# Kernel tuning notes

Hardware: AMD Instinct MI355X
Metric: run time of the kernel (lower is better)

## Reference

```python
import jax, jax.numpy as jnp
import numpy as np
import math

EMBED = 1024
HEADS = 16
HEAD_DIM = EMBED // HEADS


def setup_inputs() -> dict:
    key = jax.random.key(0)
    ks = jax.random.split(key, 9)
    B, S = 2, 2048
    query = jax.random.normal(ks[0], (B, S, EMBED), dtype=jnp.float32)
    key_t = jax.random.normal(ks[1], (B, S, EMBED), dtype=jnp.float32)
    value = jax.random.normal(ks[2], (B, S, EMBED), dtype=jnp.float32)
    mask = jax.random.randint(ks[3], (B, 1, S, S), 0, 2, dtype=jnp.int32)
    # nn.Linear(head_dim, head_dim, bias=False) weights: [out, in]
    sc = 1.0 / math.sqrt(HEAD_DIM)
    Wq = jax.random.uniform(ks[4], (HEAD_DIM, HEAD_DIM), jnp.float32, -sc, sc)
    Wk = jax.random.uniform(ks[5], (HEAD_DIM, HEAD_DIM), jnp.float32, -sc, sc)
    Wv = jax.random.uniform(ks[6], (HEAD_DIM, HEAD_DIM), jnp.float32, -sc, sc)
    so = 1.0 / math.sqrt(EMBED)
    Wo = jax.random.uniform(ks[7], (EMBED, EMBED), jnp.float32, -so, so)
    bo = jax.random.uniform(ks[8], (EMBED,), jnp.float32, -so, so)
    return {"query": query, "key": key_t, "value": value, "mask": mask,
            "Wq": Wq, "Wk": Wk, "Wv": Wv, "Wo": Wo, "bo": bo}


def reference(query, key, value, mask, Wq, Wk, Wv, Wo, bo):
    B, Sq, E = query.shape
    Sk = key.shape[1]
    H, D = HEADS, HEAD_DIM
    # Faithful raw reshape into heads (as in the torch source, no transpose)
    q = query.reshape(B, H, Sq, D)
    k = key.reshape(B, H, Sk, D)
    v = value.reshape(B, H, Sk, D)
    # per-head_dim Linear (bias-free): x @ W.T
    Q = jnp.einsum('bhsd,ed->bhse', q, Wq)
    K = jnp.einsum('bhsd,ed->bhse', k, Wk)
    V = jnp.einsum('bhsd,ed->bhse', v, Wv)
    scores = jnp.einsum('bhqd,bhkd->bhqk', Q, K)  # [B,H,Sq,Sk]
    scores = jnp.where(mask == 0, jnp.float32(-1e20), scores)
    # NOTE: source divides by sqrt(embed_size), not sqrt(head_dim)
    attn = jax.nn.softmax(scores / jnp.float32(math.sqrt(E)), axis=-1)
    out = jnp.einsum('bhqk,bhkd->bhqd', attn, V).reshape(B, Sq, H * D)
    return out @ Wo.T + bo
```

## Files before the change

kernel.cpp:

```cpp
#include <hip/hip_runtime.h>

typedef __attribute__((ext_vector_type(8))) short short8;
typedef __attribute__((ext_vector_type(4))) float f32x4;
typedef __attribute__((ext_vector_type(2))) int int2v;
typedef __attribute__((ext_vector_type(4))) int int4v;

__device__ __forceinline__ short f2bf(float f) {
  unsigned u = __builtin_bit_cast(unsigned, f);
  u += 0x7fff + ((u >> 16) & 1);
  return (short)(u >> 16);
}

__device__ __forceinline__ int pk2bf(float lo, float hi) {
#if defined(__gfx950__) && __has_builtin(__builtin_amdgcn_cvt_pk_bf16_f32)
  typedef __attribute__((ext_vector_type(2))) __bf16 bf16x2;
  bf16x2 v = __builtin_amdgcn_cvt_pk_bf16_f32(lo, hi);
  return __builtin_bit_cast(int, v);
#else
  return (int)(unsigned short)(short)f2bf(lo) | (((int)f2bf(hi)) << 16);
#endif
}

__device__ __forceinline__ short8 pack8(f32x4 a, f32x4 b) {
  int4v t;
  t.x = pk2bf(a[0], a[1]);
  t.y = pk2bf(a[2], a[3]);
  t.z = pk2bf(b[0], b[1]);
  t.w = pk2bf(b[2], b[3]);
  return __builtin_bit_cast(short8, t);
}

__device__ __forceinline__ float fand(float p, int m) {
  return __builtin_bit_cast(float, __builtin_bit_cast(int, p) & m);
}

__device__ __forceinline__ int bmask(unsigned nib, int bit) {
#if __has_builtin(__builtin_amdgcn_sbfe)
  return __builtin_amdgcn_sbfe((int)nib, bit, 1);
#else
  return -(int)((nib >> bit) & 1);
#endif
}

__device__ __forceinline__ float fexp2(float x) {
#if __has_builtin(__builtin_amdgcn_exp2f)
  return __builtin_amdgcn_exp2f(x);
#else
  return exp2f(x);
#endif
}

__device__ __forceinline__ void glds16(const short* g, short* lbase, int lane) {
#if __has_builtin(__builtin_amdgcn_global_load_lds)
  __builtin_amdgcn_global_load_lds(
      (const __attribute__((address_space(1))) unsigned int*)g,
      (__attribute__((address_space(3))) unsigned int*)lbase, 16, 0, 0);
#else
  *(short8*)(lbase + lane * 8) = *(const short8*)g;
#endif
}

__global__ __launch_bounds__(256) void prep(const float* __restrict__ q,
                                            const float* __restrict__ k,
                                            const float* __restrict__ v,
                                            const float* __restrict__ Wq,
                                            const float* __restrict__ Wk,
                                            const float* __restrict__ Wv,
                                            const float* __restrict__ Wo,
                                            const int* __restrict__ mask,
                                            short* __restrict__ Qp,
                                            short* __restrict__ Kp,
                                            short* __restrict__ Vtp,
                                            short* __restrict__ Wob,
                                            unsigned long long* __restrict__ mpk) {
  const int bid = blockIdx.x;
  const int tid = threadIdx.x;

  if (bid >= 4096) {
#pragma unroll
    for (int it = 0; it < 4; ++it) {
      const int gid = ((bid - 4096) * 4 + it) * 256 + tid;
      const int base = gid & ~63, j = gid & 63;
      const int val = mask[base + ((j & 3) << 4) + (j >> 2)];
      const unsigned long long bal = __ballot(val != 0);
      if (j == 0) mpk[gid >> 6] = bal;
    }
    return;
  }
  if (bid >= 3072) {
    const int i = ((bid - 3072) * 256 + tid) * 4;
    const f32x4 x = *(const f32x4*)&Wo[i];
    int2v o;
    o.x = pk2bf(x[0], x[1]);
    o.y = pk2bf(x[2], x[3]);
    *(int2v*)&Wob[i] = o;
    return;
  }

  __shared__ short xt[64][72];
  __shared__ short ot[64][72];
  const int mode = bid >> 10;
  const int bt = bid & 1023;
  const float* X;
  const float* W;
  float scale;
  if (mode == 0) { X = q; W = Wq; scale = 0.045084220f; }
  else if (mode == 1) { X = k; W = Wk; scale = 1.0f; }
  else { X = v; W = Wv; scale = 1.0f; }

  const int r0 = bt * 64;
  const int row = tid >> 2, seg = (tid & 3) * 16;
  const f32x4* xs = (const f32x4*)(X + (r0 + row) * 64 + seg);
  const f32x4 x0 = xs[0], x1 = xs[1], x2 = xs[2], x3 = xs[3];
  *(short8*)&xt[row][seg] = pack8(x0, x1);
  *(short8*)&xt[row][seg + 8] = pack8(x2, x3);
  __syncthreads();

  const int lane = tid & 63, wave = tid >> 6;
  const int m16 = lane & 15, quad = lane >> 4;

  const short8 a0 = *(const short8*)&xt[wave * 16 + m16][quad * 8];
  const short8 a1 = *(const short8*)&xt[wave * 16 + m16][32 + quad * 8];

  f32x4 acc[4];
#pragma unroll
  for (int nt = 0; nt < 4; ++nt) {
    const f32x4* wp0 = (const f32x4*)&W[(nt * 16 + m16) * 64 + quad * 8];
    const f32x4* wp1 = (const f32x4*)&W[(nt * 16 + m16) * 64 + 32 + quad * 8];
    const short8 b0 = pack8(wp0[0], wp0[1]);
    const short8 b1 = pack8(wp1[0], wp1[1]);
    f32x4 z = (f32x4){0.f, 0.f, 0.f, 0.f};
    z = __builtin_amdgcn_mfma_f32_16x16x32_bf16(a0, b0, z, 0, 0, 0);
    z = __builtin_amdgcn_mfma_f32_16x16x32_bf16(a1, b1, z, 0, 0, 0);
    acc[nt] = z;
  }

  if (mode != 2) {
#pragma unroll
    for (int nt = 0; nt < 4; ++nt)
#pragma unroll
      for (int r = 0; r < 4; ++r)
        ot[wave * 16 + quad * 4 + r][nt * 16 + m16] = f2bf(acc[nt][r] * scale);
  } else {
#pragma unroll
    for (int nt = 0; nt < 4; ++nt)
#pragma unroll
      for (int r = 0; r < 4; ++r)
        ot[nt * 16 + m16][16 * quad + 4 * r + wave] = f2bf(acc[nt][r]);
  }
  __syncthreads();

  const int orow = tid >> 2, opart = tid & 3;
  if (mode != 2) {
    short* dst = (mode == 0 ? Qp : Kp) + (r0 + orow) * 64 + opart * 16;
    *(short8*)&dst[0] = *(const short8*)&ot[orow][opart * 16];
    *(short8*)&dst[8] = *(const short8*)&ot[orow][opart * 16 + 8];
  } else {
    const int bh = r0 >> 11, s0 = r0 & 2047;
    short* dst = Vtp + bh * 131072 + orow * 2048 + s0 + opart * 16;
    *(short8*)&dst[0] = *(const short8*)&ot[orow][opart * 16];
    *(short8*)&dst[8] = *(const short8*)&ot[orow][opart * 16 + 8];
  }
}

__global__ __launch_bounds__(512) void flash2(const short* __restrict__ Qp,
                                              const short* __restrict__ Kp,
                                              const short* __restrict__ Vt,
                                              const unsigned long long* __restrict__ mpk,
                                              short* __restrict__ O) {
  __shared__ __attribute__((aligned(16))) short kv[4][4096];
  __shared__ __attribute__((aligned(16))) short pt[2][128][72];
  __shared__ float lbuf[128];
  const int tid = threadIdx.x;
  const int bid = blockIdx.x;
  const int local = bid >> 3;
  const int bh = (bid & 7) * 4 + (local >> 4);
  const int q0 = (local & 15) << 7;
  const int b = bh >> 4;
  const short* Qh = Qp + bh * 131072;
  const short* Kh = Kp + bh * 131072;
  const short* Vh = Vt + bh * 131072;
  const int lane = tid & 63, wave = tid >> 6;
  const int half = wave >> 2, wq = wave & 3;
  const int m16 = lane & 15, quad = lane >> 4;
  const int srow = lane >> 3, sj = (lane & 7) ^ srow;
  const int msh = m16 * 4;
  const int koff = m16 * 128 + ((quad ^ (m16 & 7)) * 16);
  short* ktb = &kv[half * 2][0];
  short* vtb = &kv[half * 2 + 1][0];
  const int tsel = wq >> 1, rbase = (wq & 1) * 32;

  short8 aq[2][2];
#pragma unroll
  for (int g = 0; g < 2; ++g)
#pragma unroll
    for (int h = 0; h < 2; ++h)
      aq[g][h] = *(const short8*)&Qh[(q0 + wq * 32 + g * 16 + m16) * 64 + h * 32 + quad * 8];

  const unsigned long long* mq = mpk + (b * 2048 + q0 + wq * 32 + quad * 4) * 32;

  float l[2][4];
  f32x4 oacc[2][4];
#pragma unroll
  for (int g = 0; g < 2; ++g)
#pragma unroll
    for (int r = 0; r < 4; ++r) l[g][r] = 0.f;
#pragma unroll
  for (int g = 0; g < 2; ++g)
#pragma unroll
    for (int dt = 0; dt < 4; ++dt) oacc[g][dt] = (f32x4){0.f, 0.f, 0.f, 0.f};

  for (int i = 0; i < 16; ++i) {
    const int ka = half * 16 + i;
    const int k0 = ka << 6;
    __syncthreads();
#pragma unroll
    for (int t = 0; t < 4; ++t) {
      const int crow = rbase + t * 8;
      if (tsel == 0)
        glds16(Kh + (k0 + crow + srow) * 64 + sj * 8, ktb + crow * 64, lane);
      else
        glds16(Vh + (crow + srow) * 2048 + k0 + sj * 8, vtb + crow * 64, lane);
    }
    __syncthreads();

    f32x4 s[2][4];
#pragma unroll
    for (int nt = 0; nt < 4; ++nt) {
      const int o0 = nt * 2048 + koff;
      const short8 kb0 = *(const short8*)((const char*)ktb + o0);
      const short8 kb1 = *(const short8*)((const char*)ktb + (o0 ^ 64));
#pragma unroll
      for (int g = 0; g < 2; ++g) {
        f32x4 z = (f32x4){0.f, 0.f, 0.f, 0.f};
        z = __builtin_amdgcn_mfma_f32_16x16x32_bf16(aq[g][0], kb0, z, 0, 0, 0);
        z = __builtin_amdgcn_mfma_f32_16x16x32_bf16(aq[g][1], kb1, z, 0, 0, 0);
        s[g][nt] = z;
      }
    }

#pragma unroll
    for (int g = 0; g < 2; ++g) {
#pragma unroll
      for (int r = 0; r < 4; ++r) {
        const unsigned long long w = mq[g * 512 + r * 32 + ka];
        const unsigned nib = (unsigned)(w >> msh) & 15u;
        const float p0 = fand(fexp2(s[g][0][r]), bmask(nib, 0));
        const float p1 = fand(fexp2(s[g][1][r]), bmask(nib, 1));
        const float p2 = fand(fexp2(s[g][2][r]), bmask(nib, 2));
        const float p3 = fand(fexp2(s[g][3][r]), bmask(nib, 3));
        l[g][r] += (p0 + p1) + (p2 + p3);
        int2v pp;
        pp.x = pk2bf(p0, p1);
        pp.y = pk2bf(p2, p3);
        *(int2v*)&pt[half][wq * 32 + g * 16 + quad * 4 + r][msh] = pp;
      }
    }

    short8 ap[2][2];
#pragma unroll
    for (int g = 0; g < 2; ++g)
#pragma unroll
      for (int h = 0; h < 2; ++h)
        ap[g][h] = *(const short8*)&pt[half][wq * 32 + g * 16 + m16][h * 32 + quad * 8];

#pragma unroll
    for (int dt = 0; dt < 4; ++dt) {
      const int o0 = dt * 2048 + koff;
      const short8 vb0 = *(const short8*)((const char*)vtb + o0);
      const short8 vb1 = *(const short8*)((const char*)vtb + (o0 ^ 64));
#pragma unroll
      for (int g = 0; g < 2; ++g) {
        f32x4 z = oacc[g][dt];
        z = __builtin_amdgcn_mfma_f32_16x16x32_bf16(ap[g][0], vb0, z, 0, 0, 0);
        z = __builtin_amdgcn_mfma_f32_16x16x32_bf16(ap[g][1], vb1, z, 0, 0, 0);
        oacc[g][dt] = z;
      }
    }
  }

#pragma unroll
  for (int g = 0; g < 2; ++g)
#pragma unroll
    for (int r = 0; r < 4; ++r)
#pragma unroll
      for (int off = 1; off < 16; off <<= 1) l[g][r] += __shfl_xor(l[g][r], off, 16);

  __syncthreads();

  if (half == 1) {
    float* obuf = (float*)kv;
#pragma unroll
    for (int g = 0; g < 2; ++g)
#pragma unroll
      for (int r = 0; r < 4; ++r) {
        const int row = wq * 32 + g * 16 + quad * 4 + r;
#pragma unroll
        for (int dt = 0; dt < 4; ++dt) obuf[row * 64 + dt * 16 + m16] = oacc[g][dt][r];
        if (m16 == 0) lbuf[row] = l[g][r];
      }
  }
  __syncthreads();

  if (half == 0) {
    const float* obuf = (const float*)kv;
#pragma unroll
    for (int g = 0; g < 2; ++g)
#pragma unroll
      for (int r = 0; r < 4; ++r) {
        const int row = wq * 32 + g * 16 + quad * 4 + r;
        const float inv = 1.0f / (l[g][r] + lbuf[row]);
#pragma unroll
        for (int dt = 0; dt < 4; ++dt)
          pt[0][row][dt * 16 + m16] =
              f2bf((oacc[g][dt][r] + obuf[row * 64 + dt * 16 + m16]) * inv);
      }
    const int orow = lane >> 1, opart = lane & 1;
    const int prow = wq * 32 + orow;
    short* og = O + (bh * 2048 + q0 + prow) * 64 + opart * 32;
#pragma unroll
    for (int c = 0; c < 32; c += 8)
      *(short8*)&og[c] = *(const short8*)&pt[0][prow][opart * 32 + c];
  }
}

__global__ __launch_bounds__(256) void outproj(const short* __restrict__ Ob,
                                               const short* __restrict__ Wob,
                                               const float* __restrict__ bo,
                                               float* __restrict__ out) {
  __shared__ short at[64][72];
  __shared__ short bt[128][72];
  const int tid = threadIdx.x;
  const int bid = blockIdx.x;
  const int ct = bid >> 6, rt = bid & 63;
  const int r0 = rt * 64, c0 = ct * 128;
  const int lane = tid & 63, wave = tid >> 6;
  const int mr = (wave >> 1) * 32, nc = (wave & 1) * 64;
  const int m16 = lane & 15, quad = lane >> 4;
  const int arow = tid >> 2, apart = tid & 3;
  const int brow = tid >> 1, bhalf = (tid & 1) * 32;

  f32x4 acc[2][4];
#pragma unroll
  for (int mt = 0; mt < 2; ++mt)
#pragma unroll
    for (int nt = 0; nt < 4; ++nt) acc[mt][nt] = (f32x4){0.f, 0.f, 0.f, 0.f};

  for (int kc = 0; kc < 16; ++kc) {
    __syncthreads();
    const short* ag = &Ob[(r0 + arow) * 1024 + kc * 64 + apart * 16];
    const short* bg = &Wob[(c0 + brow) * 1024 + kc * 64 + bhalf];
    *(short8*)&at[arow][apart * 16] = *(const short8*)&ag[0];
    *(short8*)&at[arow][apart * 16 + 8] = *(const short8*)&ag[8];
    *(short8*)&bt[brow][bhalf] = *(const short8*)&bg[0];
    *(short8*)&bt[brow][bhalf + 8] = *(const short8*)&bg[8];
    *(short8*)&bt[brow][bhalf + 16] = *(const short8*)&bg[16];
    *(short8*)&bt[brow][bhalf + 24] = *(const short8*)&bg[24];
    __syncthreads();

#pragma unroll
    for (int kh = 0; kh < 2; ++kh) {
      short8 af[2], bf[4];
#pragma unroll
      for (int i = 0; i < 2; ++i)
        af[i] = *(const short8*)&at[mr + i * 16 + m16][kh * 32 + quad * 8];
#pragma unroll
      for (int j = 0; j < 4; ++j)
        bf[j] = *(const short8*)&bt[nc + j * 16 + m16][kh * 32 + quad * 8];
#pragma unroll
      for (int mt = 0; mt < 2; ++mt)
#pragma unroll
        for (int nt = 0; nt < 4; ++nt)
          acc[mt][nt] = __builtin_amdgcn_mfma_f32_16x16x32_bf16(af[mt], bf[nt], acc[mt][nt], 0, 0, 0);
    }
  }

#pragma unroll
  for (int nt = 0; nt < 4; ++nt) {
    const int col = c0 + nc + nt * 16 + m16;
    const float bias = bo[col];
#pragma unroll
    for (int mt = 0; mt < 2; ++mt)
#pragma unroll
      for (int rr = 0; rr < 4; ++rr)
        out[(r0 + mr + mt * 16 + quad * 4 + rr) * 1024 + col] = acc[mt][nt][rr] + bias;
  }
}

extern "C" void kernel_launch(void* const* d_in, const int* in_sizes, int n_in,
                              void* d_out, int out_size, void* d_ws, size_t ws_size,
                              hipStream_t stream) {
  const float* query = (const float*)d_in[0];
  const float* key = (const float*)d_in[1];
  const float* value = (const float*)d_in[2];
  const int* mask = (const int*)d_in[3];
  const float* Wq = (const float*)d_in[4];
  const float* Wk = (const float*)d_in[5];
  const float* Wv = (const float*)d_in[6];
  const float* Wo = (const float*)d_in[7];
  const float* bo = (const float*)d_in[8];
  float* out = (float*)d_out;

  char* ws = (char*)d_ws;
  short* Qp = (short*)(ws);
  short* Kp = (short*)(ws + 8388608);
  short* Vt = (short*)(ws + 16777216);
  short* Ob = (short*)(ws + 25165824);
  short* Wob = (short*)(ws + 33554432);
  unsigned long long* mpk = (unsigned long long*)(ws + 35651584);

  prep<<<12288, 256, 0, stream>>>(query, key, value, Wq, Wk, Wv, Wo, mask,
                                  Qp, Kp, Vt, Wob, mpk);
  flash2<<<512, 512, 0, stream>>>(Qp, Kp, Vt, mpk, Ob);
  outproj<<<512, 256, 0, stream>>>(Ob, Wob, bo, out);
}
```

Baseline: 253.4 us.

## Replace split-K flash kernel with double-buffered single-pass 256-thread version

The attention kernel no longer splits the key range across two 4-wave halves of a 512-thread block, which had to merge partial outputs and row sums through shared memory at the end. Each 4-wave block now walks all 32 key tiles itself. The next K/V tile and its mask words are prefetched into a second LDS buffer while the current tile is computed, leaving one barrier per iteration. This removes the cross-half reduction and hides load latency, at the cost of half as many waves per block and a longer serial loop per wave.

```diff
diff --git a/kernel.cpp b/kernel.cpp
--- a/kernel.cpp
+++ b/kernel.cpp
@@ -163,14 +163,14 @@
   }
 }
 
-__global__ __launch_bounds__(512) void flash2(const short* __restrict__ Qp,
+__global__ __launch_bounds__(256) void flashp(const short* __restrict__ Qp,
                                               const short* __restrict__ Kp,
                                               const short* __restrict__ Vt,
                                               const unsigned long long* __restrict__ mpk,
                                               short* __restrict__ O) {
-  __shared__ __attribute__((aligned(16))) short kv[4][4096];
-  __shared__ __attribute__((aligned(16))) short pt[2][128][72];
-  __shared__ float lbuf[128];
+  __shared__ __attribute__((aligned(16))) short kt[2][4096];
+  __shared__ __attribute__((aligned(16))) short vt[2][4096];
+  __shared__ __attribute__((aligned(16))) short pt[128][72];
   const int tid = threadIdx.x;
   const int bid = blockIdx.x;
   const int local = bid >> 3;
@@ -181,23 +181,19 @@
   const short* Kh = Kp + bh * 131072;
   const short* Vh = Vt + bh * 131072;
   const int lane = tid & 63, wave = tid >> 6;
-  const int half = wave >> 2, wq = wave & 3;
   const int m16 = lane & 15, quad = lane >> 4;
   const int srow = lane >> 3, sj = (lane & 7) ^ srow;
   const int msh = m16 * 4;
   const int koff = m16 * 128 + ((quad ^ (m16 & 7)) * 16);
-  short* ktb = &kv[half * 2][0];
-  short* vtb = &kv[half * 2 + 1][0];
-  const int tsel = wq >> 1, rbase = (wq & 1) * 32;
 
   short8 aq[2][2];
 #pragma unroll
   for (int g = 0; g < 2; ++g)
 #pragma unroll
     for (int h = 0; h < 2; ++h)
-      aq[g][h] = *(const short8*)&Qh[(q0 + wq * 32 + g * 16 + m16) * 64 + h * 32 + quad * 8];
-
-  const unsigned long long* mq = mpk + (b * 2048 + q0 + wq * 32 + quad * 4) * 32;
+      aq[g][h] = *(const short8*)&Qh[(q0 + wave * 32 + g * 16 + m16) * 64 + h * 32 + quad * 8];
+
+  const unsigned long long* mq = mpk + (b * 2048 + q0 + wave * 32 + quad * 4) * 32;
 
   float l[2][4];
   f32x4 oacc[2][4];
@@ -210,26 +206,35 @@
 #pragma unroll
     for (int dt = 0; dt < 4; ++dt) oacc[g][dt] = (f32x4){0.f, 0.f, 0.f, 0.f};
 
-  for (int i = 0; i < 16; ++i) {
-    const int ka = half * 16 + i;
-    const int k0 = ka << 6;
+  auto stage = [&](int buf, int ka) {
+#pragma unroll
+    for (int t = 0; t < 2; ++t) {
+      const int crow = wave * 16 + t * 8;
+      glds16(Kh + (ka * 64 + crow + srow) * 64 + sj * 8, &kt[buf][crow * 64], lane);
+      glds16(Vh + (crow + srow) * 2048 + ka * 64 + sj * 8, &vt[buf][crow * 64], lane);
+    }
+  };
+  auto lmask = [&](unsigned long long (&mw)[2][4], int ka) {
+#pragma unroll
+    for (int g = 0; g < 2; ++g)
+#pragma unroll
+      for (int r = 0; r < 4; ++r) mw[g][r] = mq[g * 512 + r * 32 + ka];
+  };
+
+  auto body = [&](int ka, int buf, unsigned long long (&mwU)[2][4],
+                  unsigned long long (&mwN)[2][4]) {
     __syncthreads();
-#pragma unroll
-    for (int t = 0; t < 4; ++t) {
-      const int crow = rbase + t * 8;
-      if (tsel == 0)
-        glds16(Kh + (k0 + crow + srow) * 64 + sj * 8, ktb + crow * 64, lane);
-      else
-        glds16(Vh + (crow + srow) * 2048 + k0 + sj * 8, vtb + crow * 64, lane);
-    }
-    __syncthreads();
+    if (ka < 31) {
+      stage(buf ^ 1, ka + 1);
+      lmask(mwN, ka + 1);
+    }
 
     f32x4 s[2][4];
 #pragma unroll
     for (int nt = 0; nt < 4; ++nt) {
       const int o0 = nt * 2048 + koff;
-      const short8 kb0 = *(const short8*)((const char*)ktb + o0);
-      const short8 kb1 = *(const short8*)((const char*)ktb + (o0 ^ 64));
+      const short8 kb0 = *(const short8*)((const char*)&kt[buf][0] + o0);
+      const short8 kb1 = *(const short8*)((const char*)&kt[buf][0] + (o0 ^ 64));
 #pragma unroll
       for (int g = 0; g < 2; ++g) {
         f32x4 z = (f32x4){0.f, 0.f, 0.f, 0.f};
@@ -243,8 +248,7 @@
     for (int g = 0; g < 2; ++g) {
 #pragma unroll
       for (int r = 0; r < 4; ++r) {
-        const unsigned long long w = mq[g * 512 + r * 32 + ka];
-        const unsigned nib = (unsigned)(w >> msh) & 15u;
+        const unsigned nib = (unsigned)(mwU[g][r] >> msh) & 15u;
         const float p0 = fand(fexp2(s[g][0][r]), bmask(nib, 0));
         const float p1 = fand(fexp2(s[g][1][r]), bmask(nib, 1));
         const float p2 = fand(fexp2(s[g][2][r]), bmask(nib, 2));
@@ -253,7 +257,7 @@
         int2v pp;
         pp.x = pk2bf(p0, p1);
         pp.y = pk2bf(p2, p3);
-        *(int2v*)&pt[half][wq * 32 + g * 16 + quad * 4 + r][msh] = pp;
+        *(int2v*)&pt[wave * 32 + g * 16 + quad * 4 + r][msh] = pp;
       }
     }
 
@@ -262,13 +266,13 @@
     for (int g = 0; g < 2; ++g)
 #pragma unroll
       for (int h = 0; h < 2; ++h)
-        ap[g][h] = *(const short8*)&pt[half][wq * 32 + g * 16 + m16][h * 32 + quad * 8];
+        ap[g][h] = *(const short8*)&pt[wave * 32 + g * 16 + m16][h * 32 + quad * 8];
 
 #pragma unroll
     for (int dt = 0; dt < 4; ++dt) {
       const int o0 = dt * 2048 + koff;
-      const short8 vb0 = *(const short8*)((const char*)vtb + o0);
-      const short8 vb1 = *(const short8*)((const char*)vtb + (o0 ^ 64));
+      const short8 vb0 = *(const short8*)((const char*)&vt[buf][0] + o0);
+      const short8 vb1 = *(const short8*)((const char*)&vt[buf][0] + (o0 ^ 64));
 #pragma unroll
       for (int g = 0; g < 2; ++g) {
         f32x4 z = oacc[g][dt];
@@ -277,51 +281,35 @@
         oacc[g][dt] = z;
       }
     }
+  };
+
+  unsigned long long mwA[2][4], mwB[2][4];
+  stage(0, 0);
+  lmask(mwA, 0);
+
+  for (int kk = 0; kk < 16; ++kk) {
+    body(2 * kk, 0, mwA, mwB);
+    body(2 * kk + 1, 1, mwB, mwA);
   }
 
 #pragma unroll
   for (int g = 0; g < 2; ++g)
 #pragma unroll
-    for (int r = 0; r < 4; ++r)
+    for (int r = 0; r < 4; ++r) {
 #pragma unroll
       for (int off = 1; off < 16; off <<= 1) l[g][r] += __shfl_xor(l[g][r], off, 16);
-
-  __syncthreads();
-
-  if (half == 1) {
-    float* obuf = (float*)kv;
-#pragma unroll
-    for (int g = 0; g < 2; ++g)
-#pragma unroll
-      for (int r = 0; r < 4; ++r) {
-        const int row = wq * 32 + g * 16 + quad * 4 + r;
-#pragma unroll
-        for (int dt = 0; dt < 4; ++dt) obuf[row * 64 + dt * 16 + m16] = oacc[g][dt][r];
-        if (m16 == 0) lbuf[row] = l[g][r];
-      }
-  }
-  __syncthreads();
-
-  if (half == 0) {
-    const float* obuf = (const float*)kv;
-#pragma unroll
-    for (int g = 0; g < 2; ++g)
-#pragma unroll
-      for (int r = 0; r < 4; ++r) {
-        const int row = wq * 32 + g * 16 + quad * 4 + r;
-        const float inv = 1.0f / (l[g][r] + lbuf[row]);
-#pragma unroll
-        for (int dt = 0; dt < 4; ++dt)
-          pt[0][row][dt * 16 + m16] =
-              f2bf((oacc[g][dt][r] + obuf[row * 64 + dt * 16 + m16]) * inv);
-      }
-    const int orow = lane >> 1, opart = lane & 1;
-    const int prow = wq * 32 + orow;
-    short* og = O + (bh * 2048 + q0 + prow) * 64 + opart * 32;
-#pragma unroll
-    for (int c = 0; c < 32; c += 8)
-      *(short8*)&og[c] = *(const short8*)&pt[0][prow][opart * 32 + c];
-  }
+      const float inv = 1.0f / l[g][r];
+#pragma unroll
+      for (int dt = 0; dt < 4; ++dt)
+        pt[wave * 32 + g * 16 + quad * 4 + r][dt * 16 + m16] = f2bf(oacc[g][dt][r] * inv);
+    }
+
+  const int orow = lane >> 1, opart = lane & 1;
+  const int prow = wave * 32 + orow;
+  short* og = O + (bh * 2048 + q0 + prow) * 64 + opart * 32;
+#pragma unroll
+  for (int c = 0; c < 32; c += 8)
+    *(short8*)&og[c] = *(const short8*)&pt[prow][opart * 32 + c];
 }
 
 __global__ __launch_bounds__(256) void outproj(const short* __restrict__ Ob,
@@ -411,6 +399,6 @@
 
   prep<<<12288, 256, 0, stream>>>(query, key, value, Wq, Wk, Wv, Wo, mask,
                                   Qp, Kp, Vt, Wob, mpk);
-  flash2<<<512, 512, 0, stream>>>(Qp, Kp, Vt, mpk, Ob);
+  flashp<<<512, 256, 0, stream>>>(Qp, Kp, Vt, mpk, Ob);
   outproj<<<512, 256, 0, stream>>>(Ob, Wob, bo, out);
 }
```

New measurement: 247.8 us. 2.2% less time.
